# Kernel tuning notes

Hardware: AMD Instinct MI355X
Metric: run time of the kernel (lower is better)

## Reference

```python
import jax, jax.numpy as jnp
import numpy as np

K = 24  # number of clusters (all ids in [0,K) assumed present per image)
DELTA_VAR = 1.0
DELTA_DIST = 2.0
VAR_W = 1.0
DIST_W = 1.0
REG_W = 1.0


def setup_inputs() -> dict:
    key = jax.random.key(0)
    k1, k2 = jax.random.split(key)
    data = jax.random.normal(k1, (4, 16, 512, 1024), dtype=jnp.float32)
    labels = jax.random.randint(k2, (4, 512, 1024), 0, K, dtype=jnp.int32)
    return {"data": data, "labels": labels}


def reference(data, labels):
    B, D, H, Wd = data.shape
    N = H * Wd
    # [B, N, D] points, [B*N] global segment ids (batch-offset cluster ids)
    X = jnp.transpose(data.reshape(B, D, N), (0, 2, 1)).reshape(B * N, D)
    seg = (labels.reshape(B, N) + jnp.arange(B, dtype=labels.dtype)[:, None] * K).reshape(-1)

    # per-cluster sums and counts -> centers  [B*K, D]
    sums = jax.ops.segment_sum(X, seg, num_segments=B * K)
    counts = jax.ops.segment_sum(jnp.ones((B * N,), X.dtype), seg, num_segments=B * K)
    centers_flat = sums / counts[:, None]
    centers = centers_flat.reshape(B, K, D)
    counts_bk = counts.reshape(B, K)

    # variance term: per-point hinged distance to own cluster center
    c_per_point = centers_flat[seg]                      # [B*N, D]
    pt_dist = jnp.linalg.norm(X - c_per_point, axis=1)   # [B*N]
    hv = jnp.maximum(pt_dist - DELTA_VAR, 0.0) ** 2
    var_per_cluster = jax.ops.segment_sum(hv, seg, num_segments=B * K).reshape(B, K) / counts_bk
    var_sum = var_per_cluster.sum()

    # distance term: pairwise center distances (diagonal kept, as in original,
    # contributing a constant delta_dist**2 per cluster)
    diff = centers[:, :, None, :] - centers[:, None, :, :]     # [B, K, K, D]
    sq = jnp.sum(diff * diff, axis=-1)                         # [B, K, K]
    eye = jnp.eye(K, dtype=bool)[None]
    cdist = jnp.where(eye, 0.0, jnp.sqrt(jnp.where(eye, 1.0, sq)))
    hd = jnp.maximum(DELTA_DIST - cdist, 0.0) ** 2
    dist_sum = hd.sum() / (2.0 * K * (K - 1))

    # regularization: mean center norm per image, summed over batch
    reg_sum = jnp.linalg.norm(centers, axis=2).mean(axis=1).sum()

    loss = (VAR_W * var_sum + DIST_W * dist_sum + REG_W * reg_sum) / B
    return loss
```

## Files before the change

kernel.cpp:

```cpp
#include <hip/hip_runtime.h>
#include <math.h>

#define KC 24
constexpr int D = 16;
constexpr int B = 4;
constexpr int N = 512 * 1024;
constexpr float DELTA_VAR = 1.0f;
constexpr float DELTA_DIST = 2.0f;

constexpr int REP = 8;
constexpr int RS  = KC * 17;
constexpr int CS  = 33;
constexpr int TPB = 512;
constexpr int PTS = 8192;
constexpr int NBLK = (B * N) / PTS;
constexpr int SL = 8;
constexpr int RREG = 8;
constexpr int RLDS = 4;
constexpr int WS_FLOATS = SL * (B * KC * D) + SL * (B * KC) + 64;


__device__ __forceinline__ float gldf(const float* p) {
    return __hip_atomic_load(p, __ATOMIC_RELAXED, __HIP_MEMORY_SCOPE_AGENT);
}

__device__ __forceinline__ void gsync(int* cnt, int* gen) {
    __syncthreads();
    if (threadIdx.x == 0) {
        int g = __hip_atomic_load(gen, __ATOMIC_ACQUIRE, __HIP_MEMORY_SCOPE_AGENT);
        if (__hip_atomic_fetch_add(cnt, 1, __ATOMIC_ACQ_REL, __HIP_MEMORY_SCOPE_AGENT) == NBLK - 1) {
            __hip_atomic_store(cnt, 0, __ATOMIC_RELAXED, __HIP_MEMORY_SCOPE_AGENT);
            __hip_atomic_fetch_add(gen, 1, __ATOMIC_ACQ_REL, __HIP_MEMORY_SCOPE_AGENT);
        } else {
            for (int it = 0; it < (1 << 22); ++it) {
                if (__hip_atomic_load(gen, __ATOMIC_ACQUIRE, __HIP_MEMORY_SCOPE_AGENT) != g) break;
                __builtin_amdgcn_s_sleep(8);
            }
        }
    }
    __syncthreads();
}

__global__ __launch_bounds__(TPB, 2) void k_fused(const float* __restrict__ data,
                                                  const int* __restrict__ labels,
                                                  float* __restrict__ ws,
                                                  float* __restrict__ out) {
    __shared__ float s_sum[REP * RS];
    __shared__ float s_cnt[REP * CS];
    __shared__ __align__(16) float4 s_data4[RLDS][PTS / 4];
    __shared__ float s_c[KC * 17];
    __shared__ float s_ic[KC];
    __shared__ float s_red[8];

    float* g_sums = ws;
    float* g_cnt  = ws + SL * (B * KC * D);
    float* g_varp = g_cnt + SL * (B * KC);
    int*   bar    = (int*)(g_varp + 64);

    const int t = threadIdx.x;
    const int chunk = blockIdx.x * PTS;
    const int b = chunk >> 19;
    const float* base = data + (size_t)(b * D) * N + (chunk & (N - 1));

    int4 lab[4];
#pragma unroll
    for (int i = 0; i < 4; ++i)
        lab[i] = *(const int4*)(labels + chunk + (i * TPB + t) * 4);

    float4 vr[RREG][4];
#pragma unroll
    for (int i = 0; i < 4; ++i)
        vr[0][i] = *(const float4*)(base + (i * TPB + t) * 4);

    for (int i = t; i < REP * RS; i += TPB) s_sum[i] = 0.f;
    for (int i = t; i < REP * CS; i += TPB) s_cnt[i] = 0.f;
    __syncthreads();

    const int rbase = (t & 7) * RS;
    const int cbase = (t & 7) * CS;
#pragma unroll
    for (int i = 0; i < 4; ++i) {
        atomicAdd(&s_cnt[cbase + lab[i].x], 1.f);
        atomicAdd(&s_cnt[cbase + lab[i].y], 1.f);
        atomicAdd(&s_cnt[cbase + lab[i].z], 1.f);
        atomicAdd(&s_cnt[cbase + lab[i].w], 1.f);
    }

    float4 v[2][4];
#pragma unroll
    for (int d = 0; d < D; ++d) {
        if (d + 1 < D) {
#pragma unroll
            for (int i = 0; i < 4; ++i) {
                float4 nx = *(const float4*)(base + (size_t)(d + 1) * N + (i * TPB + t) * 4);
                if (d + 1 < RREG) vr[d + 1][i] = nx;
                else              v[(d + 1) & 1][i] = nx;
            }
        }
#pragma unroll
        for (int i = 0; i < 4; ++i) {
            const float4 c = (d < RREG) ? vr[d][i] : v[d & 1][i];
            if (d >= RREG && d < RREG + RLDS) s_data4[d - RREG][i * TPB + t] = c;
            atomicAdd(&s_sum[rbase + lab[i].x * 17 + d], c.x);
            atomicAdd(&s_sum[rbase + lab[i].y * 17 + d], c.y);
            atomicAdd(&s_sum[rbase + lab[i].z * 17 + d], c.z);
            atomicAdd(&s_sum[rbase + lab[i].w * 17 + d], c.w);
        }
    }
    __syncthreads();

    const int slice = blockIdx.x & (SL - 1);
    float* gs = g_sums + slice * (B * KC * D) + b * (KC * D);
    float* gc = g_cnt  + slice * (B * KC)     + b * KC;
    const int rot = (blockIdx.x * 131) & 255;
    for (int i = t; i < KC * D; i += TPB) {
        int j = (i + rot) % (KC * D);
        int c = j >> 4, dd = j & 15;
        float s = 0.f;
#pragma unroll
        for (int r = 0; r < REP; ++r) s += s_sum[r * RS + c * 17 + dd];
        atomicAdd(&gs[j], s);
    }
    if (t < KC) {
        float s = 0.f;
#pragma unroll
        for (int r = 0; r < REP; ++r) s += s_cnt[r * CS + t];
        atomicAdd(&gc[t], s);
    }

#pragma unroll
    for (int i = 0; i < 4; ++i)
        v[0][i] = *(const float4*)(base + (size_t)(RREG + RLDS) * N + (i * TPB + t) * 4);

    gsync(bar, bar + 1);

    if (t < KC) {
        float cn = 0.f;
#pragma unroll
        for (int r = 0; r < SL; ++r) cn += gldf(&g_cnt[r * (B * KC) + b * KC + t]);
        s_ic[t] = 1.f / cn;
    }
    __syncthreads();
    for (int i = t; i < KC * D; i += TPB) {
        int c = i >> 4, dd = i & 15;
        float s = 0.f;
#pragma unroll
        for (int r = 0; r < SL; ++r) s += gldf(&g_sums[r * (B * KC * D) + b * (KC * D) + i]);
        s_c[c * 17 + dd] = s * s_ic[c];
    }
    __syncthreads();

    float ac[16];
#pragma unroll
    for (int i = 0; i < 16; ++i) ac[i] = 0.f;

#pragma unroll
    for (int d = 0; d < RREG; ++d) {
#pragma unroll
        for (int i = 0; i < 4; ++i) {
            const float4 c = vr[d][i];
            float df;
            df = c.x - s_c[lab[i].x * 17 + d]; ac[i * 4 + 0] += df * df;
            df = c.y - s_c[lab[i].y * 17 + d]; ac[i * 4 + 1] += df * df;
            df = c.z - s_c[lab[i].z * 17 + d]; ac[i * 4 + 2] += df * df;
            df = c.w - s_c[lab[i].w * 17 + d]; ac[i * 4 + 3] += df * df;
        }
    }
#pragma unroll
    for (int p = 0; p < RLDS; ++p) {
        const int d = RREG + p;
#pragma unroll
        for (int i = 0; i < 4; ++i) {
            const float4 c = s_data4[p][i * TPB + t];
            float df;
            df = c.x - s_c[lab[i].x * 17 + d]; ac[i * 4 + 0] += df * df;
            df = c.y - s_c[lab[i].y * 17 + d]; ac[i * 4 + 1] += df * df;
            df = c.z - s_c[lab[i].z * 17 + d]; ac[i * 4 + 2] += df * df;
            df = c.w - s_c[lab[i].w * 17 + d]; ac[i * 4 + 3] += df * df;
        }
    }
#pragma unroll
    for (int dd = 0; dd < D - RREG - RLDS; ++dd) {
        const int d = RREG + RLDS + dd;
        if (dd + 1 < D - RREG - RLDS) {
#pragma unroll
            for (int i = 0; i < 4; ++i)
                v[(dd + 1) & 1][i] =
                    *(const float4*)(base + (size_t)(d + 1) * N + (i * TPB + t) * 4);
        }
#pragma unroll
        for (int i = 0; i < 4; ++i) {
            const float4 c = v[dd & 1][i];
            float df;
            df = c.x - s_c[lab[i].x * 17 + d]; ac[i * 4 + 0] += df * df;
            df = c.y - s_c[lab[i].y * 17 + d]; ac[i * 4 + 1] += df * df;
            df = c.z - s_c[lab[i].z * 17 + d]; ac[i * 4 + 2] += df * df;
            df = c.w - s_c[lab[i].w * 17 + d]; ac[i * 4 + 3] += df * df;
        }
    }

    float hsum = 0.f;
#pragma unroll
    for (int i = 0; i < 4; ++i) {
        float h;
        h = fmaxf(sqrtf(ac[i * 4 + 0]) - DELTA_VAR, 0.f); hsum += h * h * s_ic[lab[i].x];
        h = fmaxf(sqrtf(ac[i * 4 + 1]) - DELTA_VAR, 0.f); hsum += h * h * s_ic[lab[i].y];
        h = fmaxf(sqrtf(ac[i * 4 + 2]) - DELTA_VAR, 0.f); hsum += h * h * s_ic[lab[i].z];
        h = fmaxf(sqrtf(ac[i * 4 + 3]) - DELTA_VAR, 0.f); hsum += h * h * s_ic[lab[i].w];
    }
    for (int o = 32; o > 0; o >>= 1) hsum += __shfl_down(hsum, o, 64);
    if ((t & 63) == 0) s_red[t >> 6] = hsum;
    __syncthreads();
    if (t == 0) {
        float s = 0.f;
#pragma unroll
        for (int w = 0; w < 8; ++w) s += s_red[w];
        atomicAdd(&g_varp[blockIdx.x & 63], s);
    }

    gsync(bar, bar + 1);

    if (blockIdx.x != 0) return;

    float* s_cF = (float*)&s_data4[0][0];
    float acc = 0.f;
    if (t < B * KC) {
        float cnt = 0.f;
#pragma unroll
        for (int r = 0; r < SL; ++r) cnt += gldf(&g_cnt[r * (B * KC) + t]);
        float ns = 0.f;
        for (int dd = 0; dd < D; ++dd) {
            float s = 0.f;
#pragma unroll
            for (int r = 0; r < SL; ++r) s += gldf(&g_sums[r * (B * KC * D) + t * D + dd]);
            float c = s / cnt;
            s_cF[t * 17 + dd] = c;
            ns += c * c;
        }
        acc = sqrtf(ns) / (float)KC;
    }
    if (t < 64) acc += gldf(&g_varp[t]);
    __syncthreads();

    float dacc = 0.f;
    for (int idx = t; idx < B * KC * KC; idx += TPB) {
        int bb = idx / (KC * KC);
        int r = idx % (KC * KC);
        int i = r / KC, j = r % KC;
        float hd;
        if (i == j) {
            hd = DELTA_DIST * DELTA_DIST;
        } else {
            const float* ci = &s_cF[(bb * KC + i) * 17];
            const float* cj = &s_cF[(bb * KC + j) * 17];
            float sq = 0.f;
            for (int dd = 0; dd < D; ++dd) { float df = ci[dd] - cj[dd]; sq += df * df; }
            float hh = fmaxf(DELTA_DIST - sqrtf(sq), 0.f);
            hd = hh * hh;
        }
        dacc += hd;
    }
    float total = acc + dacc / (2.f * KC * (KC - 1));

    for (int o = 32; o > 0; o >>= 1) total += __shfl_down(total, o, 64);
    if ((t & 63) == 0) s_red[t >> 6] = total;
    __syncthreads();
    if (t == 0) {
        float s = 0.f;
#pragma unroll
        for (int w = 0; w < 8; ++w) s += s_red[w];
        out[0] = s / (float)B;
    }
}

extern "C" void kernel_launch(void* const* d_in, const int* in_sizes, int n_in,
                              void* d_out, int out_size, void* d_ws, size_t ws_size,
                              hipStream_t stream) {
    const float* data  = (const float*)d_in[0];
    const int* labels  = (const int*)d_in[1];
    float* ws          = (float*)d_ws;

    hipMemsetAsync(d_ws, 0, WS_FLOATS * sizeof(float) + 2 * sizeof(int), stream);
    k_fused<<<NBLK, TPB, 0, stream>>>(data, labels, ws, (float*)d_out);
}
```

Measured before the change: 393.1 us.

## Keep all data in registers/LDS to eliminate second-pass global reloads

Raises register-held dimensions from 8 to 12 and stores the first 4 dimensions in LDS, so all 16 dimensions stay on-chip across the grid barrier. The second pass no longer re-reads 4 dimensions from global memory. Launch bounds drop the 2-blocks-per-CU hint to allow the extra registers, and an asm keep-alive stops the compiler from rematerialising loads. The barrier spin also sleeps for shorter intervals. The risk is higher register pressure lowering occupancy, and, because all blocks must be co-resident for the grid barrier, a possible deadlock if occupancy falls too far.

```diff
diff --git a/kernel.cpp b/kernel.cpp
--- a/kernel.cpp
+++ b/kernel.cpp
@@ -15,8 +15,8 @@
 constexpr int PTS = 8192;
 constexpr int NBLK = (B * N) / PTS;
 constexpr int SL = 8;
-constexpr int RREG = 8;
 constexpr int RLDS = 4;
+constexpr int RREG = 12;
 constexpr int WS_FLOATS = SL * (B * KC * D) + SL * (B * KC) + 64;
 
 
@@ -32,19 +32,21 @@
             __hip_atomic_store(cnt, 0, __ATOMIC_RELAXED, __HIP_MEMORY_SCOPE_AGENT);
             __hip_atomic_fetch_add(gen, 1, __ATOMIC_ACQ_REL, __HIP_MEMORY_SCOPE_AGENT);
         } else {
-            for (int it = 0; it < (1 << 22); ++it) {
+            for (int it = 0; it < (1 << 24); ++it) {
                 if (__hip_atomic_load(gen, __ATOMIC_ACQUIRE, __HIP_MEMORY_SCOPE_AGENT) != g) break;
-                __builtin_amdgcn_s_sleep(8);
+                __builtin_amdgcn_s_sleep(2);
             }
         }
     }
     __syncthreads();
 }
 
-__global__ __launch_bounds__(TPB, 2) void k_fused(const float* __restrict__ data,
-                                                  const int* __restrict__ labels,
-                                                  float* __restrict__ ws,
-                                                  float* __restrict__ out) {
+#define KEEP4(f4) asm volatile("" : "+v"((f4).x), "+v"((f4).y), "+v"((f4).z), "+v"((f4).w))
+
+__global__ __launch_bounds__(TPB) void k_fused(const float* __restrict__ data,
+                                               const int* __restrict__ labels,
+                                               float* __restrict__ ws,
+                                               float* __restrict__ out) {
     __shared__ float s_sum[REP * RS];
     __shared__ float s_cnt[REP * CS];
     __shared__ __align__(16) float4 s_data4[RLDS][PTS / 4];
@@ -67,10 +69,10 @@
     for (int i = 0; i < 4; ++i)
         lab[i] = *(const int4*)(labels + chunk + (i * TPB + t) * 4);
 
-    float4 vr[RREG][4];
+    float4 tmp[2][4];
 #pragma unroll
     for (int i = 0; i < 4; ++i)
-        vr[0][i] = *(const float4*)(base + (i * TPB + t) * 4);
+        tmp[0][i] = *(const float4*)(base + (i * TPB + t) * 4);
 
     for (int i = t; i < REP * RS; i += TPB) s_sum[i] = 0.f;
     for (int i = t; i < REP * CS; i += TPB) s_cnt[i] = 0.f;
@@ -86,27 +88,33 @@
         atomicAdd(&s_cnt[cbase + lab[i].w], 1.f);
     }
 
-    float4 v[2][4];
+    float4 vr[RREG][4];
 #pragma unroll
     for (int d = 0; d < D; ++d) {
         if (d + 1 < D) {
 #pragma unroll
             for (int i = 0; i < 4; ++i) {
                 float4 nx = *(const float4*)(base + (size_t)(d + 1) * N + (i * TPB + t) * 4);
-                if (d + 1 < RREG) vr[d + 1][i] = nx;
-                else              v[(d + 1) & 1][i] = nx;
+                if (d + 1 < RLDS) tmp[(d + 1) & 1][i] = nx;
+                else              vr[d + 1 - RLDS][i] = nx;
             }
         }
 #pragma unroll
         for (int i = 0; i < 4; ++i) {
-            const float4 c = (d < RREG) ? vr[d][i] : v[d & 1][i];
-            if (d >= RREG && d < RREG + RLDS) s_data4[d - RREG][i * TPB + t] = c;
+            const float4 c = (d < RLDS) ? tmp[d & 1][i] : vr[d - RLDS][i];
+            if (d < RLDS) s_data4[d][i * TPB + t] = c;
             atomicAdd(&s_sum[rbase + lab[i].x * 17 + d], c.x);
             atomicAdd(&s_sum[rbase + lab[i].y * 17 + d], c.y);
             atomicAdd(&s_sum[rbase + lab[i].z * 17 + d], c.z);
             atomicAdd(&s_sum[rbase + lab[i].w * 17 + d], c.w);
         }
     }
+
+#pragma unroll
+    for (int d = 0; d < RREG; ++d)
+#pragma unroll
+        for (int i = 0; i < 4; ++i) KEEP4(vr[d][i]);
+
     __syncthreads();
 
     const int slice = blockIdx.x & (SL - 1);
@@ -128,10 +136,6 @@
         atomicAdd(&gc[t], s);
     }
 
-#pragma unroll
-    for (int i = 0; i < 4; ++i)
-        v[0][i] = *(const float4*)(base + (size_t)(RREG + RLDS) * N + (i * TPB + t) * 4);
-
     gsync(bar, bar + 1);
 
     if (t < KC) {
@@ -155,20 +159,8 @@
     for (int i = 0; i < 16; ++i) ac[i] = 0.f;
 
 #pragma unroll
-    for (int d = 0; d < RREG; ++d) {
-#pragma unroll
-        for (int i = 0; i < 4; ++i) {
-            const float4 c = vr[d][i];
-            float df;
-            df = c.x - s_c[lab[i].x * 17 + d]; ac[i * 4 + 0] += df * df;
-            df = c.y - s_c[lab[i].y * 17 + d]; ac[i * 4 + 1] += df * df;
-            df = c.z - s_c[lab[i].z * 17 + d]; ac[i * 4 + 2] += df * df;
-            df = c.w - s_c[lab[i].w * 17 + d]; ac[i * 4 + 3] += df * df;
-        }
-    }
-#pragma unroll
     for (int p = 0; p < RLDS; ++p) {
-        const int d = RREG + p;
+        const int d = p;
 #pragma unroll
         for (int i = 0; i < 4; ++i) {
             const float4 c = s_data4[p][i * TPB + t];
@@ -180,17 +172,11 @@
         }
     }
 #pragma unroll
-    for (int dd = 0; dd < D - RREG - RLDS; ++dd) {
-        const int d = RREG + RLDS + dd;
-        if (dd + 1 < D - RREG - RLDS) {
-#pragma unroll
-            for (int i = 0; i < 4; ++i)
-                v[(dd + 1) & 1][i] =
-                    *(const float4*)(base + (size_t)(d + 1) * N + (i * TPB + t) * 4);
-        }
+    for (int rr = 0; rr < RREG; ++rr) {
+        const int d = RLDS + rr;
 #pragma unroll
         for (int i = 0; i < 4; ++i) {
-            const float4 c = v[dd & 1][i];
+            const float4 c = vr[rr][i];
             float df;
             df = c.x - s_c[lab[i].x * 17 + d]; ac[i * 4 + 0] += df * df;
             df = c.y - s_c[lab[i].y * 17 + d]; ac[i * 4 + 1] += df * df;
```

Measured after the change: 398.6 us. Within noise of the previous version (+1.4%).
